# Performance work log

Hardware: AMD Instinct MI355X
Metric: run time of the kernel (lower is better)

The kernel has to match this reference:

```python
import jax, jax.numpy as jnp
import numpy as np

D = 1024
N_HEAD = 16
D_HEAD = D // N_HEAD
B, S = 4, 2048
EPS = 1e-6


def rmsnorm(x, w):
    # x: [..., d_head]
    return x / jnp.sqrt(jnp.mean(x * x, axis=-1, keepdims=True) + EPS) * w


def setup_inputs() -> dict:
    key = jax.random.key(0)
    ks = jax.random.split(key, 6)
    x = jax.random.normal(ks[0], (B, S, D), dtype=jnp.float32)
    # causal mask: True means masked (upper triangle above diagonal)
    mask = jnp.triu(jnp.ones((S, S), dtype=bool), k=1)
    scale = 1.0 / np.sqrt(D)
    W_qkv = jax.random.normal(ks[1], (D, 3 * D), dtype=jnp.float32) * scale
    b_qkv = jnp.zeros((3 * D,), dtype=jnp.float32)
    W_o = jax.random.normal(ks[2], (D, D), dtype=jnp.float32) * scale
    b_o = jnp.zeros((D,), dtype=jnp.float32)
    wq = jnp.ones((D_HEAD,), dtype=jnp.float32)
    wk = jnp.ones((D_HEAD,), dtype=jnp.float32)
    return {"x": x, "mask": mask, "W_qkv": W_qkv, "b_qkv": b_qkv,
            "W_o": W_o, "b_o": b_o, "wq": wq, "wk": wk}


def reference(x, mask, W_qkv, b_qkv, W_o, b_o, wq, wk):
    b, s, d = x.shape
    qkv = x @ W_qkv + b_qkv  # [b,s,3d]
    q, k, v = jnp.split(qkv, 3, axis=-1)
    q = q.reshape(b, s, N_HEAD, D_HEAD)
    k = k.reshape(b, s, N_HEAD, D_HEAD)
    v = v.reshape(b, s, N_HEAD, D_HEAD)
    q = rmsnorm(q, wq)
    k = rmsnorm(k, wk)
    # NOTE: no 1/sqrt(d_head) scaling, faithful to the source
    attn = jnp.einsum('bqhd,bkhd->bhqk', q, k)
    attn = jnp.where(mask[None, None, :, :], -jnp.inf, attn)
    attn = jax.nn.softmax(attn, axis=-1)
    z = jnp.einsum('bhqk,bkhd->bqhd', attn, v).reshape(b, s, d)
    return z @ W_o + b_o
```

## Files before the change

kernel.cpp:

```cpp
#include <hip/hip_runtime.h>
#include <cmath>

typedef _Float16 half_t;
typedef _Float16 half8 __attribute__((ext_vector_type(8)));
typedef _Float16 half4v __attribute__((ext_vector_type(4)));
typedef float float4v __attribute__((ext_vector_type(4)));

#define LOG2E 1.44269504088896340736f

#define GLDS16(g, l)                                                                   \
    __builtin_amdgcn_global_load_lds((const __attribute__((address_space(1))) void*)(g), \
                                     (__attribute__((address_space(3))) void*)(l), 16, 0, 0)

#define BAR_LGKM() __asm__ volatile("s_waitcnt lgkmcnt(0)\n\ts_barrier" ::: "memory")
#define BAR_VM(n)  __asm__ volatile("s_waitcnt vmcnt(" #n ")\n\ts_barrier" ::: "memory")

__global__ void cast_f32_f16(const float* __restrict__ in, half_t* __restrict__ out, int n) {
    int i = (blockIdx.x * blockDim.x + threadIdx.x) * 4;
    if (i >= n) return;
    float4 v = *(const float4*)(in + i);
    half4v o;
    o[0] = (half_t)v.x; o[1] = (half_t)v.y; o[2] = (half_t)v.z; o[3] = (half_t)v.w;
    *(half4v*)(out + i) = o;
}

__global__ void transpose_cast(const float* __restrict__ in, half_t* __restrict__ out, int R, int C) {
    __shared__ float tile[32][33];
    int c0 = blockIdx.x * 32, r0 = blockIdx.y * 32;
    int tx = threadIdx.x, ty = threadIdx.y;
    for (int p = 0; p < 4; p++) {
        int r = r0 + ty + p * 8;
        tile[ty + p * 8][tx] = in[(size_t)r * C + c0 + tx];
    }
    __syncthreads();
    for (int p = 0; p < 4; p++) {
        int c = c0 + ty + p * 8;
        out[(size_t)c * R + r0 + tx] = (half_t)tile[tx][ty + p * 8];
    }
}

__global__ __launch_bounds__(512, 2) void gemm_qkv(
    const half_t* __restrict__ A,
    const half_t* __restrict__ Bt,
    const float* __restrict__ bias,
    const float* __restrict__ wq, const float* __restrict__ wk,
    half_t* __restrict__ Qh, half_t* __restrict__ Kh, half_t* __restrict__ Vt,
    int M, int N, int K)
{
    __shared__ __align__(16) half_t As[2][2][128 * 64];
    __shared__ __align__(16) half_t Bs[2][2][256 * 32];

    int t = threadIdx.x;
    int lane = t & 63, w = t >> 6;
    int lrow = lane & 15, quad = lane >> 4;
    int wm = w >> 2, wn = w & 3;

    int cpx = gridDim.x >> 3;
    int bid = blockIdx.x;
    int wg = (bid & 7) * cpx + (bid >> 3);
    int nbn = N >> 8;
    int mb = wg / nbn, nb = wg % nbn;
    int m0 = mb << 8, n0 = nb << 8;

    int ar = t >> 3;
    int ac = (t & 7) ^ (ar & 7);
    const half_t* gAbase = A + (size_t)(m0 + ar) * K + ac * 8;
    int br = t >> 2;
    int bc = ((t & 3) - (t >> 3)) & 3;
    const half_t* gBbase = Bt + (size_t)(n0 + br) * K + bc * 8;

    auto stageA = [&](int buf, int a, int T) {
        const half_t* s = gAbase + (size_t)a * 128 * K + T * 64;
        GLDS16(s,                  &As[buf][a][w * 512]);
        GLDS16(s + (size_t)64 * K, &As[buf][a][4096 + w * 512]);
    };
    auto stageB = [&](int buf, int kh, int T) {
        const half_t* s = gBbase + T * 64 + kh * 32;
        GLDS16(s,                   &Bs[buf][kh][w * 512]);
        GLDS16(s + (size_t)128 * K, &Bs[buf][kh][4096 + w * 512]);
    };

    int sw = lrow & 7;
    int cx0 = ((0 + quad) ^ sw) * 8;
    int cx1 = ((4 + quad) ^ sw) * 8;
    int posq = (quad + (lrow >> 1)) & 3;
    int aoffs = (wm * 64 + lrow) * 64;
    int boffs = (wn * 64 + lrow) * 32 + posq * 8;

    half8 af0[4], af1[4];
    half8 b0[4], b1[4];
    float4v acc[2][4][4] = {};

    auto loadAk = [&](int buf, int a, int cx, half8 (&dst)[4]) {
        #pragma unroll
        for (int mi = 0; mi < 4; mi++)
            dst[mi] = *(const half8*)(&As[buf][a][aoffs + mi * 1024 + cx]);
    };
    auto loadBf = [&](int buf, int kh, half8 (&dst)[4]) {
        #pragma unroll
        for (int ni = 0; ni < 4; ni++)
            dst[ni] = *(const half8*)(&Bs[buf][kh][boffs + ni * 512]);
    };

#define MFMA16(AF, BF, AI)                                                        \
    do { _Pragma("unroll")                                                        \
        for (int mi = 0; mi < 4; mi++) { _Pragma("unroll")                        \
            for (int ni = 0; ni < 4; ni++)                                        \
                acc[AI][mi][ni] = __builtin_amdgcn_mfma_f32_16x16x32_f16(         \
                    AF[mi], BF[ni], acc[AI][mi][ni], 0, 0, 0);                    \
        } } while (0)

#define PH_TOP()                                                   \
    do {                                                           \
        __asm__ volatile("s_waitcnt lgkmcnt(0)" ::: "memory");     \
        __builtin_amdgcn_sched_barrier(0);                         \
    } while (0)
#define PH_BOT(STG)                                                               \
    do {                                                                          \
        __builtin_amdgcn_sched_barrier(0);                                        \
        if (STG) { __asm__ volatile("s_waitcnt vmcnt(6)" ::: "memory"); }         \
        else     { __asm__ volatile("s_waitcnt vmcnt(0)" ::: "memory"); }         \
        __asm__ volatile("s_barrier" ::: "memory");                               \
    } while (0)

    int nk = K >> 6;

    stageB(0, 0, 0); stageB(0, 1, 0); stageA(0, 0, 0); stageA(0, 1, 0);
    stageB(1, 0, 1); stageB(1, 1, 1); stageA(1, 0, 1); stageA(1, 1, 1);
    __asm__ volatile("s_waitcnt vmcnt(8)" ::: "memory");
    __asm__ volatile("s_barrier" ::: "memory");
    loadAk(0, 0, cx0, af0);
    loadBf(0, 0, b0);
    __asm__ volatile("s_waitcnt lgkmcnt(0)" ::: "memory");
    __asm__ volatile("s_barrier" ::: "memory");

    for (int T = 0; T < nk; T++) {
        int buf = T & 1, nbuf = buf ^ 1;
        bool stg = (T + 2 < nk);
        bool rdn = (T + 1 < nk);

        PH_TOP();
        loadAk(buf, 1, cx0, af1);
        loadBf(buf, 1, b1);
        if (stg) stageB(buf, 0, T + 2);
        __builtin_amdgcn_sched_barrier(0);
        __builtin_amdgcn_s_setprio(1);
        MFMA16(af0, b0, 0);
        __builtin_amdgcn_s_setprio(0);
        PH_BOT(stg);

        PH_TOP();
        loadAk(buf, 0, cx1, af0);
        if (stg) stageB(buf, 1, T + 2);
        __builtin_amdgcn_sched_barrier(0);
        __builtin_amdgcn_s_setprio(1);
        MFMA16(af1, b0, 1);
        __builtin_amdgcn_s_setprio(0);
        PH_BOT(stg);

        PH_TOP();
        loadAk(buf, 1, cx1, af1);
        if (rdn) loadBf(nbuf, 0, b0);
        if (stg) stageA(buf, 0, T + 2);
        __builtin_amdgcn_sched_barrier(0);
        __builtin_amdgcn_s_setprio(1);
        MFMA16(af0, b1, 0);
        __builtin_amdgcn_s_setprio(0);
        PH_BOT(stg);

        PH_TOP();
        if (rdn) loadAk(nbuf, 0, cx0, af0);
        if (stg) stageA(buf, 1, T + 2);
        __builtin_amdgcn_sched_barrier(0);
        __builtin_amdgcn_s_setprio(1);
        MFMA16(af1, b1, 1);
        __builtin_amdgcn_s_setprio(0);
        PH_BOT(stg);
    }

    int nglob = n0 + wn * 64;
    if (nglob < 2048) {
        int isK = nglob >> 10;
        int h = (nglob >> 6) & 15;
        const float* wv = isK ? wk : wq;
        half_t* dst = isK ? Kh : Qh;
        float post = isK ? 1.0f : LOG2E;
        #pragma unroll
        for (int a = 0; a < 2; a++) {
            #pragma unroll
            for (int mi = 0; mi < 4; mi++) {
                #pragma unroll
                for (int r = 0; r < 4; r++) {
                    int gr = m0 + a * 128 + wm * 64 + mi * 16 + quad * 4 + r;
                    float v[4]; float ss = 0.f;
                    #pragma unroll
                    for (int ni = 0; ni < 4; ni++) {
                        v[ni] = acc[a][mi][ni][r] + bias[nglob + ni * 16 + lrow];
                        ss += v[ni] * v[ni];
                    }
                    ss += __shfl_xor(ss, 1);
                    ss += __shfl_xor(ss, 2);
                    ss += __shfl_xor(ss, 4);
                    ss += __shfl_xor(ss, 8);
                    float rr = rsqrtf(ss * (1.0f / 64.0f) + 1e-6f) * post;
                    int bb = gr >> 11, s = gr & 2047;
                    size_t rowbase = ((size_t)((bb * 16 + h) * 2048 + s)) * 64;
                    #pragma unroll
                    for (int ni = 0; ni < 4; ni++) {
                        int d = ni * 16 + lrow;
                        dst[rowbase + d] = (half_t)(v[ni] * rr * wv[d]);
                    }
                }
            }
        }
    } else {
        #pragma unroll
        for (int a = 0; a < 2; a++) {
            #pragma unroll
            for (int mi = 0; mi < 4; mi++) {
                int gr = m0 + a * 128 + wm * 64 + mi * 16 + quad * 4;
                int bb = gr >> 11, s = gr & 2047;
                #pragma unroll
                for (int ni = 0; ni < 4; ni++) {
                    int dg = nglob + ni * 16 + lrow - 2048;
                    float bv = bias[nglob + ni * 16 + lrow];
                    half4v oh;
                    #pragma unroll
                    for (int r = 0; r < 4; r++) oh[r] = (half_t)(acc[a][mi][ni][r] + bv);
                    *(half4v*)(Vt + ((size_t)((bb * 16 + (dg >> 6)) * 64 + (dg & 63))) * 2048 + s) = oh;
                }
            }
        }
    }
#undef PH_TOP
#undef PH_BOT
#undef MFMA16
}

template <int MODE>
__global__ __launch_bounds__(256, 3) void gemm_f16(
    const half_t* __restrict__ A,
    const half_t* __restrict__ Bt,
    const float* __restrict__ bias,
    void* __restrict__ Cout,
    int M, int N, int K,
    const float* __restrict__ wq, const float* __restrict__ wk,
    half_t* __restrict__ Qh, half_t* __restrict__ Kh)
{
    __shared__ __align__(16) half_t As[3][128 * 32];
    __shared__ __align__(16) half_t Bs[3][128 * 32];
    int t = threadIdx.x;
    int lane = t & 63, w = t >> 6;
    int m0 = blockIdx.x * 128, n0 = blockIdx.y * 128;
    int wm = (w >> 1) * 64, wn = (w & 1) * 64;
    int lrow = lane & 15, quad = lane >> 4;

    int lc = ((t & 3) - (t >> 3)) & 3;
    const half_t* gA = A  + (size_t)(m0 + (t >> 2)) * K + lc * 8;
    const half_t* gB = Bt + (size_t)(n0 + (t >> 2)) * K + lc * 8;
    half_t* ldsA[3] = { &As[0][w * 512], &As[1][w * 512], &As[2][w * 512] };
    half_t* ldsB[3] = { &Bs[0][w * 512], &Bs[1][w * 512], &Bs[2][w * 512] };

    int posq = (quad + (lrow >> 1)) & 3;

    float4v acc[4][4] = {};

    GLDS16(gA,                       ldsA[0]);
    GLDS16(gA + (size_t)64 * K,      ldsA[0] + 2048);
    GLDS16(gB,                       ldsB[0]);
    GLDS16(gB + (size_t)64 * K,      ldsB[0] + 2048);
    GLDS16(gA + 32,                  ldsA[1]);
    GLDS16(gA + (size_t)64 * K + 32, ldsA[1] + 2048);
    GLDS16(gB + 32,                  ldsB[1]);
    GLDS16(gB + (size_t)64 * K + 32, ldsB[1] + 2048);

    int nk = K >> 5;
    for (int ki = 0; ki < nk; ki++) {
        int cur = ki % 3, pre = (ki + 2) % 3;
        BAR_LGKM();
        if (ki + 2 < nk) {
            int kp = (ki + 2) << 5;
            GLDS16(gA + kp,                  ldsA[pre]);
            GLDS16(gA + (size_t)64 * K + kp, ldsA[pre] + 2048);
            GLDS16(gB + kp,                  ldsB[pre]);
            GLDS16(gB + (size_t)64 * K + kp, ldsB[pre] + 2048);
            BAR_VM(8);
        } else if (ki + 1 < nk) {
            BAR_VM(4);
        } else {
            BAR_VM(0);
        }
        half8 af[4], bf[4];
        for (int i = 0; i < 4; i++) af[i] = *(const half8*)(&As[cur][(wm + i * 16 + lrow) * 32 + posq * 8]);
        for (int i = 0; i < 4; i++) bf[i] = *(const half8*)(&Bs[cur][(wn + i * 16 + lrow) * 32 + posq * 8]);
        for (int mi = 0; mi < 4; mi++)
            for (int ni = 0; ni < 4; ni++)
                acc[mi][ni] = __builtin_amdgcn_mfma_f32_16x16x32_f16(af[mi], bf[ni], acc[mi][ni], 0, 0, 0);
    }

    if (MODE == 0) {
        float* out = (float*)Cout;
        for (int mi = 0; mi < 4; mi++)
            for (int ni = 0; ni < 4; ni++)
                for (int r = 0; r < 4; r++) {
                    int gr = m0 + wm + mi * 16 + quad * 4 + r;
                    int gc = n0 + wn + ni * 16 + lrow;
                    out[(size_t)gr * N + gc] = acc[mi][ni][r] + bias[gc];
                }
    } else {
        int nglob = n0 + wn;
        if (nglob < 2048) {
            int isK = nglob >> 10;
            int h = (nglob >> 6) & 15;
            const float* wv = isK ? wk : wq;
            half_t* dst = isK ? Kh : Qh;
            float post = isK ? 1.0f : LOG2E;
            for (int mi = 0; mi < 4; mi++)
                for (int r = 0; r < 4; r++) {
                    int gr = m0 + wm + mi * 16 + quad * 4 + r;
                    float v[4]; float ss = 0.f;
                    for (int ni = 0; ni < 4; ni++) {
                        v[ni] = acc[mi][ni][r] + bias[nglob + ni * 16 + lrow];
                        ss += v[ni] * v[ni];
                    }
                    ss += __shfl_xor(ss, 1);
                    ss += __shfl_xor(ss, 2);
                    ss += __shfl_xor(ss, 4);
                    ss += __shfl_xor(ss, 8);
                    float rr = rsqrtf(ss * (1.0f / 64.0f) + 1e-6f) * post;
                    int bb = gr >> 11, s = gr & 2047;
                    size_t rowbase = ((size_t)((bb * 16 + h) * 2048 + s)) * 64;
                    for (int ni = 0; ni < 4; ni++) {
                        int d = ni * 16 + lrow;
                        dst[rowbase + d] = (half_t)(v[ni] * rr * wv[d]);
                    }
                }
        } else {
            half_t* Vt = (half_t*)Cout;
            for (int mi = 0; mi < 4; mi++) {
                int gr = m0 + wm + mi * 16 + quad * 4;
                int bb = gr >> 11, s = gr & 2047;
                for (int ni = 0; ni < 4; ni++) {
                    int dg = nglob + ni * 16 + lrow - 2048;
                    float bv = bias[nglob + ni * 16 + lrow];
                    half4v oh;
                    for (int r = 0; r < 4; r++) oh[r] = (half_t)(acc[mi][ni][r] + bv);
                    *(half4v*)(Vt + ((size_t)((bb * 16 + (dg >> 6)) * 64 + (dg & 63))) * 2048 + s) = oh;
                }
            }
        }
    }
}

__global__ __launch_bounds__(512, 4) void attn(
    const half_t* __restrict__ Qh, const half_t* __restrict__ Kh, const half_t* __restrict__ Vt,
    half_t* __restrict__ Z)
{
    __shared__ __align__(16) half_t Ks[2][128 * 64];
    __shared__ __align__(16) half_t Vs[2][64 * 128];
    __shared__ __align__(16) half_t Ps[8][16 * 64];

    int bh = blockIdx.x;
    int b = bh >> 4, h = bh & 15;
    int t = threadIdx.x, lane = t & 63, w = t >> 6;
    int lrow = lane & 15, quad = lane >> 4;

    int scc = (lane & 7) ^ ((lane >> 3) & 7);
    const half_t* gK0 = Kh + ((size_t)bh * 2048 + w * 16 + (lane >> 3)) * 64 + scc * 8;
    int vr0 = w * 8 + (lane >> 4);
    int vc0 = (lane & 15) ^ (lane >> 4);
    int vc1 = (lane & 15) ^ ((lane >> 4) + 4);
    const half_t* gV0 = Vt + ((size_t)bh * 64 + vr0) * 2048 + vc0 * 8;
    const half_t* gV1 = Vt + ((size_t)bh * 64 + vr0 + 4) * 2048 + vc1 * 8;
    half_t* ldsK[2] = { &Ks[0][w * 1024], &Ks[1][w * 1024] };
    half_t* ldsV[2] = { &Vs[0][w * 1024], &Vs[1][w * 1024] };

    int sw = lrow & 7;
    int cA = (quad ^ sw) * 8;
    int cB = ((quad + 4) ^ sw) * 8;
    half_t* PsW = &Ps[w][lrow * 64];

    for (int pass = 0; pass < 2; pass++) {
        int qt = pass ? (15 - (int)blockIdx.y) : (int)blockIdx.y;
        int q0w = qt * 128 + w * 16;

        const half_t* Qbase = Qh + ((size_t)bh * 2048 + q0w + lrow) * 64;
        half8 qf0 = *(const half8*)(Qbase + quad * 8);
        half8 qf1 = *(const half8*)(Qbase + 32 + quad * 8);

        float4v ot[4] = {};
        float m = -__builtin_inff(), l = 0.f;

        int nt = qt + 1;
        __syncthreads();
        GLDS16(gK0,       ldsK[0]);
        GLDS16(gK0 + 512, ldsK[0] + 512);
        GLDS16(gV0,       ldsV[0]);
        GLDS16(gV1,       ldsV[0] + 512);

        for (int kt = 0; kt < nt; kt++) {
            int cur = kt & 1, nxt = cur ^ 1;
            int kb = kt * 128;
            BAR_LGKM();
            if (kt + 1 < nt) {
                size_t ko = (size_t)(kb + 128);
                GLDS16(gK0 + ko * 64,       ldsK[nxt]);
                GLDS16(gK0 + ko * 64 + 512, ldsK[nxt] + 512);
                GLDS16(gV0 + ko,            ldsV[nxt]);
                GLDS16(gV1 + ko,            ldsV[nxt] + 512);
                BAR_VM(4);
            } else {
                BAR_VM(0);
            }

            float4v st[8];
            for (int f = 0; f < 8; f++) {
                float4v z = {};
                const half_t* kr = &Ks[cur][(f * 16 + lrow) * 64];
                half8 k0 = *(const half8*)(kr + cA);
                half8 k1 = *(const half8*)(kr + cB);
                z = __builtin_amdgcn_mfma_f32_16x16x32_f16(k0, qf0, z, 0, 0, 0);
                z = __builtin_amdgcn_mfma_f32_16x16x32_f16(k1, qf1, z, 0, 0, 0);
                st[f] = z;
            }
            if (kb + 127 > q0w) {
                int qabs = q0w + lrow;
                for (int f = 0; f < 8; f++)
                    for (int r = 0; r < 4; r++) {
                        int key = kb + f * 16 + quad * 4 + r;
                        if (key > qabs) st[f][r] = -__builtin_inff();
                    }
            }
            float tm = st[0][0];
            for (int f = 0; f < 8; f++)
                for (int r = 0; r < 4; r++) tm = fmaxf(tm, st[f][r]);
            tm = fmaxf(tm, __shfl_xor(tm, 16));
            tm = fmaxf(tm, __shfl_xor(tm, 32));
            float mn = fmaxf(m, tm);
            float alpha = __builtin_amdgcn_exp2f(m - mn);
            m = mn;
            float rs = 0.f;
            uint2 pw1[4];
            for (int f = 0; f < 8; f++) {
                float p0 = __builtin_amdgcn_exp2f(st[f][0] - mn);
                float p1 = __builtin_amdgcn_exp2f(st[f][1] - mn);
                float p2 = __builtin_amdgcn_exp2f(st[f][2] - mn);
                float p3 = __builtin_amdgcn_exp2f(st[f][3] - mn);
                rs += (p0 + p1) + (p2 + p3);
                uint2 pw;
                pw.x = __builtin_bit_cast(unsigned, __builtin_amdgcn_cvt_pkrtz(p0, p1));
                pw.y = __builtin_bit_cast(unsigned, __builtin_amdgcn_cvt_pkrtz(p2, p3));
                if (f < 4) {
                    int cc = (2 * f + (quad >> 1)) ^ sw;
                    *(uint2*)(PsW + cc * 8 + (quad & 1) * 4) = pw;
                } else {
                    pw1[f - 4] = pw;
                }
            }
            rs += __shfl_xor(rs, 16);
            rs += __shfl_xor(rs, 32);
            l = l * alpha + rs;
            for (int f2 = 0; f2 < 4; f2++)
                for (int r = 0; r < 4; r++) ot[f2][r] *= alpha;

            __asm__ volatile("s_waitcnt lgkmcnt(0)" ::: "memory");
            half8 p0v = *(const half8*)(PsW + cA);
            half8 p1v = *(const half8*)(PsW + cB);
            for (int f2 = 0; f2 < 4; f2++) {
                int row = f2 * 16 + lrow;
                half8 v0 = *(const half8*)(&Vs[cur][row * 128 + ((quad ^ sw)) * 8]);
                half8 v1 = *(const half8*)(&Vs[cur][row * 128 + (((4 + quad) ^ sw)) * 8]);
                ot[f2] = __builtin_amdgcn_mfma_f32_16x16x32_f16(v0, p0v, ot[f2], 0, 0, 0);
                ot[f2] = __builtin_amdgcn_mfma_f32_16x16x32_f16(v1, p1v, ot[f2], 0, 0, 0);
            }
            for (int f = 0; f < 4; f++) {
                int cc = (2 * f + (quad >> 1)) ^ sw;
                *(uint2*)(PsW + cc * 8 + (quad & 1) * 4) = pw1[f];
            }
            __asm__ volatile("s_waitcnt lgkmcnt(0)" ::: "memory");
            half8 p2v = *(const half8*)(PsW + cA);
            half8 p3v = *(const half8*)(PsW + cB);
            for (int f2 = 0; f2 < 4; f2++) {
                int row = f2 * 16 + lrow;
                half8 v2 = *(const half8*)(&Vs[cur][row * 128 + (((8 + quad) ^ sw)) * 8]);
                half8 v3 = *(const half8*)(&Vs[cur][row * 128 + (((12 + quad) ^ sw)) * 8]);
                ot[f2] = __builtin_amdgcn_mfma_f32_16x16x32_f16(v2, p2v, ot[f2], 0, 0, 0);
                ot[f2] = __builtin_amdgcn_mfma_f32_16x16x32_f16(v3, p3v, ot[f2], 0, 0, 0);
            }
        }

        float inv = 1.0f / l;
        size_t base = ((size_t)(b * 2048) + q0w + lrow) * 1024 + h * 64;
        for (int f2 = 0; f2 < 4; f2++) {
            half4v oh;
            for (int r = 0; r < 4; r++) oh[r] = (half_t)(ot[f2][r] * inv);
            *(half4v*)(Z + base + f2 * 16 + quad * 4) = oh;
        }
    }
}

extern "C" void kernel_launch(void* const* d_in, const int* in_sizes, int n_in,
                              void* d_out, int out_size, void* d_ws, size_t ws_size,
                              hipStream_t stream)
{
    const float* x     = (const float*)d_in[0];
    const float* W_qkv = (const float*)d_in[2];
    const float* b_qkv = (const float*)d_in[3];
    const float* W_o   = (const float*)d_in[4];
    const float* b_o   = (const float*)d_in[5];
    const float* wq    = (const float*)d_in[6];
    const float* wk    = (const float*)d_in[7];
    float* out = (float*)d_out;

    char* ws = (char*)d_ws;
    half_t* xh   = (half_t*)(ws);
    half_t* Wqt  = (half_t*)(ws + (16ull << 20));
    half_t* Wot  = (half_t*)(ws + (22ull << 20));
    half_t* Qh   = (half_t*)(ws + (40ull << 20));
    half_t* Kh   = (half_t*)(ws + (56ull << 20));
    half_t* Vt   = (half_t*)(ws + (72ull << 20));
    half_t* zh   = xh;

    cast_f32_f16<<<8192, 256, 0, stream>>>(x, xh, 8192 * 1024);
    transpose_cast<<<dim3(96, 32), dim3(32, 8), 0, stream>>>(W_qkv, Wqt, 1024, 3072);
    transpose_cast<<<dim3(32, 32), dim3(32, 8), 0, stream>>>(W_o, Wot, 1024, 1024);
    gemm_qkv<<<384, 512, 0, stream>>>(xh, Wqt, b_qkv, wq, wk, Qh, Kh, Vt, 8192, 3072, 1024);
    attn<<<dim3(64, 8), 512, 0, stream>>>(Qh, Kh, Vt, zh);
    gemm_f16<0><<<dim3(64, 8), 256, 0, stream>>>(zh, Wot, b_o, out, 8192, 1024, 1024,
                                                 nullptr, nullptr, nullptr, nullptr);
}
```

Measured before the change: 273.3 us.

## Shrink QKV GEMM tile to 128x256 with two-phase K pipeline

The QKV projection GEMM tile drops from 256x256 to 128x256 rows per workgroup, doubling the grid to 768 blocks and halving the accumulator registers. The A tile now uses the same 32-wide k-half layout as B instead of a 64-wide XOR-swizzled layout, and the inner loop becomes two phases per 64-wide K step with prefetch one stage ahead. The aim is better occupancy and more blocks across CUs, at the cost of less reuse of B per block and more global traffic for the weight matrix.

```diff
diff --git a/kernel.cpp b/kernel.cpp
--- a/kernel.cpp
+++ b/kernel.cpp
@@ -47,7 +47,7 @@
     half_t* __restrict__ Qh, half_t* __restrict__ Kh, half_t* __restrict__ Vt,
     int M, int N, int K)
 {
-    __shared__ __align__(16) half_t As[2][2][128 * 64];
+    __shared__ __align__(16) half_t As[2][2][128 * 32];
     __shared__ __align__(16) half_t Bs[2][2][256 * 32];
 
     int t = threadIdx.x;
@@ -60,54 +60,47 @@
     int wg = (bid & 7) * cpx + (bid >> 3);
     int nbn = N >> 8;
     int mb = wg / nbn, nb = wg % nbn;
-    int m0 = mb << 8, n0 = nb << 8;
-
-    int ar = t >> 3;
-    int ac = (t & 7) ^ (ar & 7);
-    const half_t* gAbase = A + (size_t)(m0 + ar) * K + ac * 8;
-    int br = t >> 2;
+    int m0 = mb << 7, n0 = nb << 8;
+
+    int sr = t >> 2;
     int bc = ((t & 3) - (t >> 3)) & 3;
-    const half_t* gBbase = Bt + (size_t)(n0 + br) * K + bc * 8;
-
-    auto stageA = [&](int buf, int a, int T) {
-        const half_t* s = gAbase + (size_t)a * 128 * K + T * 64;
-        GLDS16(s,                  &As[buf][a][w * 512]);
-        GLDS16(s + (size_t)64 * K, &As[buf][a][4096 + w * 512]);
+    const half_t* gAbase = A  + (size_t)(m0 + sr) * K + bc * 8;
+    const half_t* gBbase = Bt + (size_t)(n0 + sr) * K + bc * 8;
+
+    auto stageA = [&](int buf, int kk, int T) {
+        GLDS16(gAbase + T * 64 + kk * 32, &As[buf][kk][w * 512]);
     };
-    auto stageB = [&](int buf, int kh, int T) {
-        const half_t* s = gBbase + T * 64 + kh * 32;
-        GLDS16(s,                   &Bs[buf][kh][w * 512]);
-        GLDS16(s + (size_t)128 * K, &Bs[buf][kh][4096 + w * 512]);
+    auto stageB = [&](int buf, int kk, int T) {
+        const half_t* s = gBbase + T * 64 + kk * 32;
+        GLDS16(s,                   &Bs[buf][kk][w * 512]);
+        GLDS16(s + (size_t)128 * K, &Bs[buf][kk][4096 + w * 512]);
     };
 
-    int sw = lrow & 7;
-    int cx0 = ((0 + quad) ^ sw) * 8;
-    int cx1 = ((4 + quad) ^ sw) * 8;
     int posq = (quad + (lrow >> 1)) & 3;
-    int aoffs = (wm * 64 + lrow) * 64;
+    int aoffs = (wm * 64 + lrow) * 32 + posq * 8;
     int boffs = (wn * 64 + lrow) * 32 + posq * 8;
 
     half8 af0[4], af1[4];
     half8 b0[4], b1[4];
-    float4v acc[2][4][4] = {};
-
-    auto loadAk = [&](int buf, int a, int cx, half8 (&dst)[4]) {
+    float4v acc[4][4] = {};
+
+    auto loadA = [&](int buf, int kk, half8 (&dst)[4]) {
         #pragma unroll
         for (int mi = 0; mi < 4; mi++)
-            dst[mi] = *(const half8*)(&As[buf][a][aoffs + mi * 1024 + cx]);
+            dst[mi] = *(const half8*)(&As[buf][kk][aoffs + mi * 512]);
     };
-    auto loadBf = [&](int buf, int kh, half8 (&dst)[4]) {
+    auto loadB = [&](int buf, int kk, half8 (&dst)[4]) {
         #pragma unroll
         for (int ni = 0; ni < 4; ni++)
-            dst[ni] = *(const half8*)(&Bs[buf][kh][boffs + ni * 512]);
+            dst[ni] = *(const half8*)(&Bs[buf][kk][boffs + ni * 512]);
     };
 
-#define MFMA16(AF, BF, AI)                                                        \
+#define MFMA16(AF, BF)                                                            \
     do { _Pragma("unroll")                                                        \
         for (int mi = 0; mi < 4; mi++) { _Pragma("unroll")                        \
             for (int ni = 0; ni < 4; ni++)                                        \
-                acc[AI][mi][ni] = __builtin_amdgcn_mfma_f32_16x16x32_f16(         \
-                    AF[mi], BF[ni], acc[AI][mi][ni], 0, 0, 0);                    \
+                acc[mi][ni] = __builtin_amdgcn_mfma_f32_16x16x32_f16(             \
+                    AF[mi], BF[ni], acc[mi][ni], 0, 0, 0);                        \
         } } while (0)
 
 #define PH_TOP()                                                   \
@@ -118,64 +111,46 @@
 #define PH_BOT(STG)                                                               \
     do {                                                                          \
         __builtin_amdgcn_sched_barrier(0);                                        \
-        if (STG) { __asm__ volatile("s_waitcnt vmcnt(6)" ::: "memory"); }         \
+        if (STG) { __asm__ volatile("s_waitcnt vmcnt(3)" ::: "memory"); }         \
         else     { __asm__ volatile("s_waitcnt vmcnt(0)" ::: "memory"); }         \
         __asm__ volatile("s_barrier" ::: "memory");                               \
     } while (0)
 
     int nk = K >> 6;
 
-    stageB(0, 0, 0); stageB(0, 1, 0); stageA(0, 0, 0); stageA(0, 1, 0);
-    stageB(1, 0, 1); stageB(1, 1, 1); stageA(1, 0, 1); stageA(1, 1, 1);
-    __asm__ volatile("s_waitcnt vmcnt(8)" ::: "memory");
+    stageA(0, 0, 0); stageB(0, 0, 0);
+    stageA(0, 1, 0); stageB(0, 1, 0);
+    stageA(1, 0, 1); stageB(1, 0, 1);
+    __asm__ volatile("s_waitcnt vmcnt(3)" ::: "memory");
     __asm__ volatile("s_barrier" ::: "memory");
-    loadAk(0, 0, cx0, af0);
-    loadBf(0, 0, b0);
+    loadA(0, 0, af0);
+    loadB(0, 0, b0);
     __asm__ volatile("s_waitcnt lgkmcnt(0)" ::: "memory");
     __asm__ volatile("s_barrier" ::: "memory");
 
     for (int T = 0; T < nk; T++) {
         int buf = T & 1, nbuf = buf ^ 1;
-        bool stg = (T + 2 < nk);
-        bool rdn = (T + 1 < nk);
+        bool s0 = (T + 1 < nk);
+        bool s1 = (T + 2 < nk);
 
         PH_TOP();
-        loadAk(buf, 1, cx0, af1);
-        loadBf(buf, 1, b1);
-        if (stg) stageB(buf, 0, T + 2);
+        loadA(buf, 1, af1);
+        loadB(buf, 1, b1);
+        if (s0) { stageA(nbuf, 1, T + 1); stageB(nbuf, 1, T + 1); }
         __builtin_amdgcn_sched_barrier(0);
         __builtin_amdgcn_s_setprio(1);
-        MFMA16(af0, b0, 0);
+        MFMA16(af0, b0);
         __builtin_amdgcn_s_setprio(0);
-        PH_BOT(stg);
+        PH_BOT(s0);
 
         PH_TOP();
-        loadAk(buf, 0, cx1, af0);
-        if (stg) stageB(buf, 1, T + 2);
+        if (s0) { loadA(nbuf, 0, af0); loadB(nbuf, 0, b0); }
+        if (s1) { stageA(buf, 0, T + 2); stageB(buf, 0, T + 2); }
         __builtin_amdgcn_sched_barrier(0);
         __builtin_amdgcn_s_setprio(1);
-        MFMA16(af1, b0, 1);
+        MFMA16(af1, b1);
         __builtin_amdgcn_s_setprio(0);
-        PH_BOT(stg);
-
-        PH_TOP();
-        loadAk(buf, 1, cx1, af1);
-        if (rdn) loadBf(nbuf, 0, b0);
-        if (stg) stageA(buf, 0, T + 2);
-        __builtin_amdgcn_sched_barrier(0);
-        __builtin_amdgcn_s_setprio(1);
-        MFMA16(af0, b1, 0);
-        __builtin_amdgcn_s_setprio(0);
-        PH_BOT(stg);
-
-        PH_TOP();
-        if (rdn) loadAk(nbuf, 0, cx0, af0);
-        if (stg) stageA(buf, 1, T + 2);
-        __builtin_amdgcn_sched_barrier(0);
-        __builtin_amdgcn_s_setprio(1);
-        MFMA16(af1, b1, 1);
-        __builtin_amdgcn_s_setprio(0);
-        PH_BOT(stg);
+        PH_BOT(s1);
     }
 
     int nglob = n0 + wn * 64;
@@ -186,49 +161,43 @@
         half_t* dst = isK ? Kh : Qh;
         float post = isK ? 1.0f : LOG2E;
         #pragma unroll
-        for (int a = 0; a < 2; a++) {
+        for (int mi = 0; mi < 4; mi++) {
             #pragma unroll
-            for (int mi = 0; mi < 4; mi++) {
+            for (int r = 0; r < 4; r++) {
+                int gr = m0 + wm * 64 + mi * 16 + quad * 4 + r;
+                float v[4]; float ss = 0.f;
                 #pragma unroll
-                for (int r = 0; r < 4; r++) {
-                    int gr = m0 + a * 128 + wm * 64 + mi * 16 + quad * 4 + r;
-                    float v[4]; float ss = 0.f;
-                    #pragma unroll
-                    for (int ni = 0; ni < 4; ni++) {
-                        v[ni] = acc[a][mi][ni][r] + bias[nglob + ni * 16 + lrow];
-                        ss += v[ni] * v[ni];
-                    }
-                    ss += __shfl_xor(ss, 1);
-                    ss += __shfl_xor(ss, 2);
-                    ss += __shfl_xor(ss, 4);
-                    ss += __shfl_xor(ss, 8);
-                    float rr = rsqrtf(ss * (1.0f / 64.0f) + 1e-6f) * post;
-                    int bb = gr >> 11, s = gr & 2047;
-                    size_t rowbase = ((size_t)((bb * 16 + h) * 2048 + s)) * 64;
-                    #pragma unroll
-                    for (int ni = 0; ni < 4; ni++) {
-                        int d = ni * 16 + lrow;
-                        dst[rowbase + d] = (half_t)(v[ni] * rr * wv[d]);
-                    }
+                for (int ni = 0; ni < 4; ni++) {
+                    v[ni] = acc[mi][ni][r] + bias[nglob + ni * 16 + lrow];
+                    ss += v[ni] * v[ni];
+                }
+                ss += __shfl_xor(ss, 1);
+                ss += __shfl_xor(ss, 2);
+                ss += __shfl_xor(ss, 4);
+                ss += __shfl_xor(ss, 8);
+                float rr = rsqrtf(ss * (1.0f / 64.0f) + 1e-6f) * post;
+                int bb = gr >> 11, s = gr & 2047;
+                size_t rowbase = ((size_t)((bb * 16 + h) * 2048 + s)) * 64;
+                #pragma unroll
+                for (int ni = 0; ni < 4; ni++) {
+                    int d = ni * 16 + lrow;
+                    dst[rowbase + d] = (half_t)(v[ni] * rr * wv[d]);
                 }
             }
         }
     } else {
         #pragma unroll
-        for (int a = 0; a < 2; a++) {
+        for (int mi = 0; mi < 4; mi++) {
+            int gr = m0 + wm * 64 + mi * 16 + quad * 4;
+            int bb = gr >> 11, s = gr & 2047;
             #pragma unroll
-            for (int mi = 0; mi < 4; mi++) {
-                int gr = m0 + a * 128 + wm * 64 + mi * 16 + quad * 4;
-                int bb = gr >> 11, s = gr & 2047;
+            for (int ni = 0; ni < 4; ni++) {
+                int dg = nglob + ni * 16 + lrow - 2048;
+                float bv = bias[nglob + ni * 16 + lrow];
+                half4v oh;
                 #pragma unroll
-                for (int ni = 0; ni < 4; ni++) {
-                    int dg = nglob + ni * 16 + lrow - 2048;
-                    float bv = bias[nglob + ni * 16 + lrow];
-                    half4v oh;
-                    #pragma unroll
-                    for (int r = 0; r < 4; r++) oh[r] = (half_t)(acc[a][mi][ni][r] + bv);
-                    *(half4v*)(Vt + ((size_t)((bb * 16 + (dg >> 6)) * 64 + (dg & 63))) * 2048 + s) = oh;
-                }
+                for (int r = 0; r < 4; r++) oh[r] = (half_t)(acc[mi][ni][r] + bv);
+                *(half4v*)(Vt + ((size_t)((bb * 16 + (dg >> 6)) * 64 + (dg & 63))) * 2048 + s) = oh;
             }
         }
     }
@@ -524,7 +493,7 @@
     cast_f32_f16<<<8192, 256, 0, stream>>>(x, xh, 8192 * 1024);
     transpose_cast<<<dim3(96, 32), dim3(32, 8), 0, stream>>>(W_qkv, Wqt, 1024, 3072);
     transpose_cast<<<dim3(32, 32), dim3(32, 8), 0, stream>>>(W_o, Wot, 1024, 1024);
-    gemm_qkv<<<384, 512, 0, stream>>>(xh, Wqt, b_qkv, wq, wk, Qh, Kh, Vt, 8192, 3072, 1024);
+    gemm_qkv<<<768, 512, 0, stream>>>(xh, Wqt, b_qkv, wq, wk, Qh, Kh, Vt, 8192, 3072, 1024);
     attn<<<dim3(64, 8), 512, 0, stream>>>(Qh, Kh, Vt, zh);
     gemm_f16<0><<<dim3(64, 8), 256, 0, stream>>>(zh, Wot, b_o, out, 8192, 1024, 1024,
                                                  nullptr, nullptr, nullptr, nullptr);
```

New measurement: 274.0 us. About the same (+0.2%).
